# Kernel tuning notes

Hardware: AMD Instinct MI355X
Metric: run time of the kernel (lower is better)

The kernel has to match this reference:

```python
import jax, jax.numpy as jnp
import numpy as np

N_NODES = 50000
N_EDGES = 600000
F_IN = 64
N_GRAPHS = 2000
OUT_DIM = 1
BN_EPS = 1e-5


def _bn(x, gamma, beta):
    # BatchNorm1d training-mode forward: biased batch stats over node/row dim
    m = jnp.mean(x, axis=0)
    v = jnp.var(x, axis=0)
    return (x - m) * jax.lax.rsqrt(v + BN_EPS) * gamma + beta


def _gcn(x, W, b, src, dst):
    # PyG GCNConv: h = x @ W; symmetric-normalized aggregation with self-loops; bias after agg
    n = x.shape[0]
    h = x @ W                                    # [N, C_out]
    ones = jnp.ones((src.shape[0],), h.dtype)
    deg = jax.ops.segment_sum(ones, dst, num_segments=n) + 1.0  # +1 self-loop
    dinv = jax.lax.rsqrt(deg)
    norm = (dinv[src] * dinv[dst])[:, None]      # [E, 1]
    agg = jax.ops.segment_sum(h[src] * norm, dst, num_segments=n)
    agg = agg + h * (1.0 / deg)[:, None]         # self-loop term: deg^{-1/2}*deg^{-1/2}
    return agg + b


def _pool_mean(x, batch, g):
    s = jax.ops.segment_sum(x, batch, num_segments=g)
    c = jax.ops.segment_sum(jnp.ones((x.shape[0],), x.dtype), batch, num_segments=g)
    return s / jnp.maximum(c, 1.0)[:, None]


def _forward(xc, xs, W1c, b1c, g1c, be1c, W2c, b2c, g2c, be2c,
             W1s, b1s, g1s, be1s, W2s, b2s, g2s, be2s,
             Wf1, bf1, gf1, bef1, Wf2, bf2,
             src_c, dst_c, src_s, dst_s, batch):
    hc = jax.nn.relu(_bn(_gcn(xc, W1c, b1c, src_c, dst_c), g1c, be1c))
    hc = jax.nn.relu(_bn(_gcn(hc, W2c, b2c, src_c, dst_c), g2c, be2c))
    hs = jax.nn.relu(_bn(_gcn(xs, W1s, b1s, src_s, dst_s), g1s, be1s))
    hs = jax.nn.relu(_bn(_gcn(hs, W2s, b2s, src_s, dst_s), g2s, be2s))
    pc = _pool_mean(hc, batch, N_GRAPHS)         # [G, 64]
    ps = _pool_mean(hs, batch, N_GRAPHS)         # [G, 64]
    h = jnp.concatenate([pc, ps], axis=1)        # [G, 128]
    h = jax.nn.relu(_bn(h @ Wf1 + bf1, gf1, bef1))  # dropout is identity in eval
    return h @ Wf2 + bf2                         # [G, OUT_DIM]


def setup_inputs() -> dict:
    key = jax.random.key(0)
    ks = jax.random.split(key, 16)

    def glorot(k, fan_in, fan_out):
        s = np.sqrt(2.0 / (fan_in + fan_out)).astype(np.float32)
        return jax.random.normal(k, (fan_in, fan_out), jnp.float32) * s

    inp = {
        'x_chromophore': jax.random.normal(ks[0], (N_NODES, F_IN), jnp.float32),
        'x_solvent': jax.random.normal(ks[1], (N_NODES, F_IN), jnp.float32),
        'edge_index_chromophore': jax.random.randint(ks[2], (2, N_EDGES), 0, N_NODES),
        'edge_index_solvent': jax.random.randint(ks[3], (2, N_EDGES), 0, N_NODES),
        'batch': jnp.sort(jax.random.randint(ks[4], (N_NODES,), 0, N_GRAPHS)),
        # chromophore branch params
        'W1c': glorot(ks[5], F_IN, 128), 'b1c': jnp.zeros((128,), jnp.float32),
        'g1c': jnp.ones((128,), jnp.float32), 'be1c': jnp.zeros((128,), jnp.float32),
        'W2c': glorot(ks[6], 128, 64), 'b2c': jnp.zeros((64,), jnp.float32),
        'g2c': jnp.ones((64,), jnp.float32), 'be2c': jnp.zeros((64,), jnp.float32),
        # solvent branch params
        'W1s': glorot(ks[7], F_IN, 128), 'b1s': jnp.zeros((128,), jnp.float32),
        'g1s': jnp.ones((128,), jnp.float32), 'be1s': jnp.zeros((128,), jnp.float32),
        'W2s': glorot(ks[8], 128, 64), 'b2s': jnp.zeros((64,), jnp.float32),
        'g2s': jnp.ones((64,), jnp.float32), 'be2s': jnp.zeros((64,), jnp.float32),
        # MLP head
        'Wf1': glorot(ks[9], 128, 64), 'bf1': jnp.zeros((64,), jnp.float32),
        'gf1': jnp.ones((64,), jnp.float32), 'bef1': jnp.zeros((64,), jnp.float32),
        'Wf2': glorot(ks[10], 64, OUT_DIM), 'bf2': jnp.zeros((OUT_DIM,), jnp.float32),
    }
    return inp


def reference(x_chromophore, x_solvent, edge_index_chromophore, edge_index_solvent, batch,
              W1c, b1c, g1c, be1c, W2c, b2c, g2c, be2c,
              W1s, b1s, g1s, be1s, W2s, b2s, g2s, be2s,
              Wf1, bf1, gf1, bef1, Wf2, bf2):
    src_c, dst_c = edge_index_chromophore[0], edge_index_chromophore[1]
    src_s, dst_s = edge_index_solvent[0], edge_index_solvent[1]
    return _forward(x_chromophore, x_solvent,
                    W1c, b1c, g1c, be1c, W2c, b2c, g2c, be2c,
                    W1s, b1s, g1s, be1s, W2s, b2s, g2s, be2s,
                    Wf1, bf1, gf1, bef1, Wf2, bf2,
                    src_c, dst_c, src_s, dst_s, batch)
```

## Files before the change

kernel.cpp:

```cpp
#include <hip/hip_runtime.h>
#include <hip/hip_bf16.h>
#include <cstdint>
#include <cstddef>

#define NN 50000
#define NE 600000
#define NG 2000
#define NBUCK 49
#define SLOTS 16
#define NCHUNK 3125

typedef __attribute__((ext_vector_type(8))) short bf8;
typedef __attribute__((ext_vector_type(4))) float f32x4;

__device__ __forceinline__ unsigned short f2bf(float f) {
    uint32_t u = __float_as_uint(f);
    uint32_t r = (u + 0x7FFFu + ((u >> 16) & 1u)) >> 16;
    return (unsigned short)r;
}
__device__ __forceinline__ float bf2f(unsigned short h) {
    return __uint_as_float(((uint32_t)h) << 16);
}
__device__ __forceinline__ float lo16(uint32_t v) { return __uint_as_float(v << 16); }
__device__ __forceinline__ float hi16(uint32_t v) { return __uint_as_float(v & 0xFFFF0000u); }

__global__ __launch_bounds__(256) void conv_bf16_kernel(const float* __restrict__ x0,
                                                        const float* __restrict__ x1,
                                                        unsigned short* __restrict__ out) {
    int b = blockIdx.y;
    const float* x = b ? x1 : x0;
    unsigned short* o = out + (size_t)b * NN * 64;
    int i = (blockIdx.x * 256 + threadIdx.x) * 4;
    if (i + 3 < NN * 64) {
        float4 v = *(const float4*)&x[i];
        ushort4 r = make_ushort4(f2bf(v.x), f2bf(v.y), f2bf(v.z), f2bf(v.w));
        *(ushort4*)&o[i] = r;
    }
}

template<int K, int N>
__global__ __launch_bounds__(256) void pack_w(const float* __restrict__ W0,
                                              const float* __restrict__ W1,
                                              unsigned short* __restrict__ out) {
    int b = blockIdx.y;
    const float* W = b ? W1 : W0;
    unsigned short* o = out + (size_t)b * K * N;
    int idx = blockIdx.x * 256 + threadIdx.x;
    const int total = (N / 16) * (K / 32) * 64;
    if (idx >= total) return;
    int l = idx & 63;
    int th = idx >> 6;
    int h = th % (K / 32);
    int t = th / (K / 32);
    int col = t * 16 + (l & 15);
    int k0 = h * 32 + (l >> 4) * 8;
    ushort4 lo = make_ushort4(f2bf(W[(k0 + 0) * N + col]), f2bf(W[(k0 + 1) * N + col]),
                              f2bf(W[(k0 + 2) * N + col]), f2bf(W[(k0 + 3) * N + col]));
    ushort4 hi = make_ushort4(f2bf(W[(k0 + 4) * N + col]), f2bf(W[(k0 + 5) * N + col]),
                              f2bf(W[(k0 + 6) * N + col]), f2bf(W[(k0 + 7) * N + col]));
    *(ushort4*)&o[idx * 8] = lo;
    *(ushort4*)&o[idx * 8 + 4] = hi;
}

__global__ __launch_bounds__(256) void bucket_hist(const int* __restrict__ d0,
                                                   const int* __restrict__ d1,
                                                   int* __restrict__ bucketCnt, int nE) {
    int b = blockIdx.y;
    const int* dst = b ? d1 : d0;
    __shared__ int h[NBUCK];
    for (int i = threadIdx.x; i < NBUCK; i += 256) h[i] = 0;
    __syncthreads();
    for (int e = blockIdx.x * 256 + threadIdx.x; e < nE; e += gridDim.x * 256)
        atomicAdd(&h[dst[e] >> 10], 1);
    __syncthreads();
    for (int i = threadIdx.x; i < NBUCK; i += 256)
        if (h[i]) atomicAdd(&bucketCnt[b * NBUCK + i], h[i]);
}

__global__ void bucket_scan(const int* __restrict__ bucketCnt,
                            int* __restrict__ bucketOff, int* __restrict__ bucketCur) {
    int b = threadIdx.x;
    if (b < 2) {
        int run = 0;
        for (int i = 0; i < NBUCK; ++i) {
            bucketOff[b * NBUCK + i] = run;
            bucketCur[b * NBUCK + i] = run;
            run += bucketCnt[b * NBUCK + i];
        }
    }
}

__global__ __launch_bounds__(256) void bucket_scatter(const int* __restrict__ s0,
                                                      const int* __restrict__ d0,
                                                      const int* __restrict__ s1,
                                                      const int* __restrict__ d1,
                                                      int* __restrict__ bucketCur,
                                                      uint32_t* __restrict__ bent, int nE) {
    int b = blockIdx.y;
    const int* src = b ? s1 : s0;
    const int* dst = b ? d1 : d0;
    __shared__ int cnt[NBUCK];
    __shared__ int base[NBUCK];
    const int tid = threadIdx.x;
    for (int i = tid; i < NBUCK; i += 256) cnt[i] = 0;
    __syncthreads();

    const int e0 = blockIdx.x * 2048 + tid;
    int bk[8], slot[8];
    uint32_t pay[8];
#pragma unroll
    for (int k = 0; k < 8; ++k) {
        int e = e0 + k * 256;
        if (e < nE) {
            int d = dst[e], s = src[e];
            bk[k] = d >> 10;
            pay[k] = ((uint32_t)(d & 1023) << 16) | (uint32_t)s;
            slot[k] = atomicAdd(&cnt[bk[k]], 1);
        } else bk[k] = -1;
    }
    __syncthreads();
    for (int i = tid; i < NBUCK; i += 256) {
        int c = cnt[i];
        base[i] = c ? atomicAdd(&bucketCur[b * NBUCK + i], c) : 0;
    }
    __syncthreads();
#pragma unroll
    for (int k = 0; k < 8; ++k)
        if (bk[k] >= 0)
            bent[(size_t)b * NE + base[bk[k]] + slot[k]] = pay[k];
}

__global__ __launch_bounds__(256) void csr_build(const uint32_t* __restrict__ bent,
                                                 const int* __restrict__ bucketOff,
                                                 const int* __restrict__ bucketCnt,
                                                 int* __restrict__ row_ptr,
                                                 float* __restrict__ dinv,
                                                 uint16_t* __restrict__ perm) {
    __shared__ int lcnt[1024];
    __shared__ int lcur[1024];
    __shared__ int sscan[256];
    const int bk = blockIdx.x;
    const int b = blockIdx.y;
    const int tid = threadIdx.x;
    const int ebase = bucketOff[b * NBUCK + bk];
    const int ecnt = bucketCnt[b * NBUCK + bk];
    const int node0 = bk << 10;
    const uint32_t* be = bent + (size_t)b * NE + ebase;
    int* rp = row_ptr + b * (NN + 1);
    float* dv = dinv + (size_t)b * NN;
    uint16_t* pm = perm + (size_t)b * NE + ebase;

    for (int i = tid; i < 1024; i += 256) lcnt[i] = 0;
    __syncthreads();
    for (int i = tid; i < ecnt; i += 256) atomicAdd(&lcnt[be[i] >> 16], 1);
    __syncthreads();

    int c[4], s = 0;
#pragma unroll
    for (int j = 0; j < 4; ++j) { c[j] = lcnt[tid * 4 + j]; s += c[j]; }
    sscan[tid] = s;
    __syncthreads();
    for (int off = 1; off < 256; off <<= 1) {
        int v = (tid >= off) ? sscan[tid - off] : 0;
        __syncthreads();
        sscan[tid] += v;
        __syncthreads();
    }
    int run = sscan[tid] - s;
#pragma unroll
    for (int j = 0; j < 4; ++j) {
        int nl = tid * 4 + j;
        int g = node0 + nl;
        if (g < NN) {
            rp[g] = ebase + run;
            lcur[nl] = run;
            dv[g] = rsqrtf((float)c[j] + 1.0f);
        }
        run += c[j];
    }
    if (bk == NBUCK - 1 && tid == 0) rp[NN] = ebase + ecnt;
    __syncthreads();

    for (int i = tid; i < ecnt; i += 256) {
        uint32_t en = be[i];
        int nl = en >> 16;
        int pos = atomicAdd(&lcur[nl], 1);
        pm[pos] = (uint16_t)(en & 0xFFFFu);
    }
}

__global__ __launch_bounds__(256) void weight_fill(const uint16_t* __restrict__ perm,
                                                   const float* __restrict__ dinv,
                                                   uint32_t* __restrict__ permw, int nE) {
    int b = blockIdx.y;
    const uint16_t* pm = perm + (size_t)b * NE;
    const float* dv = dinv + (size_t)b * NN;
    uint32_t* pw = permw + (size_t)b * NE;
    int i = (blockIdx.x * 256 + threadIdx.x) * 4;
    if (i + 3 < nE) {
        ushort4 s4 = *(const ushort4*)&pm[i];
        uint4 o;
        o.x = ((uint32_t)f2bf(dv[s4.x]) << 16) | (uint32_t)s4.x;
        o.y = ((uint32_t)f2bf(dv[s4.y]) << 16) | (uint32_t)s4.y;
        o.z = ((uint32_t)f2bf(dv[s4.z]) << 16) | (uint32_t)s4.z;
        o.w = ((uint32_t)f2bf(dv[s4.w]) << 16) | (uint32_t)s4.w;
        *(uint4*)&pw[i] = o;
    } else {
        for (; i < nE; ++i) {
            uint16_t s = pm[i];
            pw[i] = ((uint32_t)f2bf(dv[s]) << 16) | (uint32_t)s;
        }
    }
}

__global__ __launch_bounds__(256) void graph_ranges(const int* __restrict__ batch,
                                                    int* __restrict__ gstart,
                                                    int* __restrict__ gend, int n) {
    int i = blockIdx.x * 256 + threadIdx.x;
    if (i >= n) return;
    int g = batch[i];
    if (i == 0 || batch[i - 1] != g) gstart[g] = i;
    if (i == n - 1 || batch[i + 1] != g) gend[g] = i + 1;
}

__global__ __launch_bounds__(256) void gemm1_mfma(const unsigned short* __restrict__ Xbf,
                                                  const unsigned short* __restrict__ Wp,
                                                  unsigned short* __restrict__ Y) {
    const int b = blockIdx.y;
    const unsigned short* __restrict__ X = Xbf + (size_t)b * NN * 64;
    const unsigned short* __restrict__ W = Wp + (size_t)b * 64 * 128;
    unsigned short* __restrict__ Yb = Y + (size_t)b * NN * 128;
    const int tid = threadIdx.x;
    const int w = tid >> 6, lane = tid & 63;
    const int chunk = blockIdx.x * 4 + w;
    if (chunk >= NCHUNK) return;
    const int m = lane & 15, quad = lane >> 4;

    const int row = chunk * 16 + m;
    bf8 a0 = *(const bf8*)&X[(size_t)row * 64 + quad * 8];
    bf8 a1 = *(const bf8*)&X[(size_t)row * 64 + 32 + quad * 8];
    f32x4 acc[8];
#pragma unroll
    for (int t = 0; t < 8; ++t) acc[t] = (f32x4){0.f, 0.f, 0.f, 0.f};
#pragma unroll
    for (int t = 0; t < 8; ++t) {
        bf8 b0 = *(const bf8*)&W[((t * 2 + 0) * 64 + lane) * 8];
        bf8 b1 = *(const bf8*)&W[((t * 2 + 1) * 64 + lane) * 8];
        acc[t] = __builtin_amdgcn_mfma_f32_16x16x32_bf16(b0, a0, acc[t], 0, 0, 0);
        acc[t] = __builtin_amdgcn_mfma_f32_16x16x32_bf16(b1, a1, acc[t], 0, 0, 0);
    }
#pragma unroll
    for (int t = 0; t < 8; ++t) {
        uint32_t lo = (uint32_t)f2bf(acc[t][0]) | ((uint32_t)f2bf(acc[t][1]) << 16);
        uint32_t hi = (uint32_t)f2bf(acc[t][2]) | ((uint32_t)f2bf(acc[t][3]) << 16);
        *(uint2*)&Yb[(size_t)row * 128 + t * 16 + quad * 4] = make_uint2(lo, hi);
    }
}

__global__ __launch_bounds__(256) void stats128_bf16(const unsigned short* __restrict__ Y,
                                                     float* __restrict__ sums) {
    const int b = blockIdx.y;
    const unsigned short* __restrict__ Yb = Y + (size_t)b * NN * 128;
    const int g = threadIdx.x & 31;
    const int rs = threadIdx.x >> 5;
    float s0 = 0.f, s1 = 0.f, s2 = 0.f, s3 = 0.f;
    float q0 = 0.f, q1 = 0.f, q2 = 0.f, q3 = 0.f;
    for (int r = blockIdx.x * 8 + rs; r < NN; r += gridDim.x * 8) {
        uint2 v = *(const uint2*)&Yb[(size_t)r * 128 + g * 4];
        float x0 = lo16(v.x);
        float x1 = hi16(v.x);
        float x2 = lo16(v.y);
        float x3 = hi16(v.y);
        s0 += x0; s1 += x1; s2 += x2; s3 += x3;
        q0 = fmaf(x0, x0, q0); q1 = fmaf(x1, x1, q1);
        q2 = fmaf(x2, x2, q2); q3 = fmaf(x3, x3, q3);
    }
    __shared__ float ls[8][128], lq[8][128];
    *(float4*)&ls[rs][g * 4] = make_float4(s0, s1, s2, s3);
    *(float4*)&lq[rs][g * 4] = make_float4(q0, q1, q2, q3);
    __syncthreads();
    if (threadIdx.x < 128) {
        const int c = threadIdx.x;
        float S = 0.f, Q = 0.f;
#pragma unroll
        for (int k = 0; k < 8; ++k) { S += ls[k][c]; Q += lq[k][c]; }
        int slot = blockIdx.x & (SLOTS - 1);
        float* sb = sums + (size_t)(b * SLOTS + slot) * 256;
        atomicAdd(&sb[c], S);
        atomicAdd(&sb[128 + c], Q);
    }
}

__global__ __launch_bounds__(256) void gemm2_mfma(const unsigned short* __restrict__ H1,
                                                  const unsigned short* __restrict__ Wp,
                                                  const float* __restrict__ sums,
                                                  const float* __restrict__ g0,
                                                  const float* __restrict__ g1,
                                                  const float* __restrict__ be0,
                                                  const float* __restrict__ be1,
                                                  unsigned short* __restrict__ Y) {
    __shared__ float scLds[128], shLds[128];
    const int b = blockIdx.y;
    const unsigned short* __restrict__ X = H1 + (size_t)b * NN * 128;
    const unsigned short* __restrict__ W = Wp + (size_t)b * 128 * 64;
    unsigned short* __restrict__ Yb = Y + (size_t)b * NN * 64;
    const int tid = threadIdx.x;

    if (tid < 128) {
        float s = 0.f, s2 = 0.f;
#pragma unroll
        for (int k = 0; k < SLOTS; ++k) {
            const float* sb = sums + (size_t)(b * SLOTS + k) * 256;
            s += sb[tid];
            s2 += sb[128 + tid];
        }
        const float invN = 1.0f / (float)NN;
        float mean = s * invN;
        float var = s2 * invN - mean * mean;
        float gamma = b ? g1[tid] : g0[tid];
        float beta = b ? be1[tid] : be0[tid];
        float sc = gamma * rsqrtf(var + 1e-5f);
        scLds[tid] = sc;
        shLds[tid] = beta - mean * sc;
    }
    __syncthreads();

    const int w = tid >> 6, lane = tid & 63;
    const int chunk = blockIdx.x * 4 + w;
    if (chunk >= NCHUNK) return;
    const int m = lane & 15, quad = lane >> 4;
    const int row = chunk * 16 + m;

    f32x4 acc[4];
#pragma unroll
    for (int t = 0; t < 4; ++t) acc[t] = (f32x4){0.f, 0.f, 0.f, 0.f};
#pragma unroll
    for (int h = 0; h < 4; ++h) {
        const int k0 = h * 32 + quad * 8;
        bf8 araw = *(const bf8*)&X[(size_t)row * 128 + k0];
        float4 sc0 = *(const float4*)&scLds[k0];
        float4 sc1 = *(const float4*)&scLds[k0 + 4];
        float4 sh0 = *(const float4*)&shLds[k0];
        float4 sh1 = *(const float4*)&shLds[k0 + 4];
        float scv[8] = {sc0.x, sc0.y, sc0.z, sc0.w, sc1.x, sc1.y, sc1.z, sc1.w};
        float shv[8] = {sh0.x, sh0.y, sh0.z, sh0.w, sh1.x, sh1.y, sh1.z, sh1.w};
        bf8 af;
#pragma unroll
        for (int j = 0; j < 8; ++j) {
            float v = bf2f((unsigned short)araw[j]);
            v = fmaxf(fmaf(v, scv[j], shv[j]), 0.f);
            af[j] = (short)f2bf(v);
        }
#pragma unroll
        for (int t = 0; t < 4; ++t) {
            bf8 bf = *(const bf8*)&W[((t * 4 + h) * 64 + lane) * 8];
            acc[t] = __builtin_amdgcn_mfma_f32_16x16x32_bf16(bf, af, acc[t], 0, 0, 0);
        }
    }
#pragma unroll
    for (int t = 0; t < 4; ++t) {
        uint32_t lo = (uint32_t)f2bf(acc[t][0]) | ((uint32_t)f2bf(acc[t][1]) << 16);
        uint32_t hi = (uint32_t)f2bf(acc[t][2]) | ((uint32_t)f2bf(acc[t][3]) << 16);
        *(uint2*)&Yb[(size_t)row * 64 + t * 16 + quad * 4] = make_uint2(lo, hi);
    }
}

template<bool STATS>
__global__ __launch_bounds__(256) void agg2_kernel(const unsigned short* __restrict__ hall,
                                                   const int* __restrict__ row_ptr,
                                                   const uint32_t* __restrict__ permw,
                                                   const float* __restrict__ dinv,
                                                   unsigned short* __restrict__ out,
                                                   float* __restrict__ sums, int nNodes) {
    const int bid = blockIdx.x;
    const int xcd = bid & 7;
    const int b = xcd >> 2;
    const int j = (bid >> 3) * 4 + (xcd & 3);
    const unsigned short* __restrict__ h = hall + (size_t)b * NN * 64;
    const int* rp = row_ptr + b * (NN + 1);
    const uint32_t* pe = permw + (size_t)b * NE;
    const float* dv = dinv + (size_t)b * NN;
    unsigned short* ob = out + (size_t)b * nNodes * 64;

    const int w = threadIdx.x >> 6;
    const int lane = threadIdx.x & 63;
    const int q = lane & 15;
    const int r = lane >> 4;
    const int d0 = j * 8 + w * 2;
    const int d1 = d0 + 1;
    const bool actA = d0 < nNodes;
    const bool actB = d1 < nNodes;

    float fA0 = 0.f, fA1 = 0.f, fA2 = 0.f, fA3 = 0.f;
    float fB0 = 0.f, fB1 = 0.f, fB2 = 0.f, fB3 = 0.f;
    int p0a = 0, p1a = 0, p0b = 0, p1b = 0;
    float dia = 0.f, dib = 0.f;
    if (actA) { p0a = rp[d0]; p1a = rp[d0 + 1]; dia = dv[d0]; }
    if (actB) { p0b = rp[d1]; p1b = rp[d1 + 1]; dib = dv[d1]; }

    float aA0 = 0.f, aA1 = 0.f, aA2 = 0.f, aA3 = 0.f;
    float aB0 = 0.f, aB1 = 0.f, aB2 = 0.f, aB3 = 0.f;
    int pa = p0a, pb = p0b;
    while (pa < p1a || pb < p1b) {
        uint32_t enA[4], enB[4];
#pragma unroll
        for (int k = 0; k < 4; ++k) {
            int e = pa + k * 4 + r;
            bool vld = e < p1a;
            enA[k] = pe[vld ? e : p0a];
            if (!vld) enA[k] &= 0xFFFFu;
        }
#pragma unroll
        for (int k = 0; k < 4; ++k) {
            int e = pb + k * 4 + r;
            bool vld = e < p1b;
            enB[k] = pe[vld ? e : p0b];
            if (!vld) enB[k] &= 0xFFFFu;
        }
#pragma unroll
        for (int k = 0; k < 4; ++k) {
            const int idx = (int)(enA[k] & 0xFFFFu);
            const float wk = __uint_as_float(enA[k] & 0xFFFF0000u);
            const uint2 hv = *(const uint2*)&h[(size_t)idx * 64 + q * 4];
            aA0 = fmaf(wk, lo16(hv.x), aA0);
            aA1 = fmaf(wk, hi16(hv.x), aA1);
            aA2 = fmaf(wk, lo16(hv.y), aA2);
            aA3 = fmaf(wk, hi16(hv.y), aA3);
        }
#pragma unroll
        for (int k = 0; k < 4; ++k) {
            const int idx = (int)(enB[k] & 0xFFFFu);
            const float wk = __uint_as_float(enB[k] & 0xFFFF0000u);
            const uint2 hv = *(const uint2*)&h[(size_t)idx * 64 + q * 4];
            aB0 = fmaf(wk, lo16(hv.x), aB0);
            aB1 = fmaf(wk, hi16(hv.x), aB1);
            aB2 = fmaf(wk, lo16(hv.y), aB2);
            aB3 = fmaf(wk, hi16(hv.y), aB3);
        }
        pa += 16;
        pb += 16;
    }
    aA0 += __shfl_xor(aA0, 16, 64); aA0 += __shfl_xor(aA0, 32, 64);
    aA1 += __shfl_xor(aA1, 16, 64); aA1 += __shfl_xor(aA1, 32, 64);
    aA2 += __shfl_xor(aA2, 16, 64); aA2 += __shfl_xor(aA2, 32, 64);
    aA3 += __shfl_xor(aA3, 16, 64); aA3 += __shfl_xor(aA3, 32, 64);
    aB0 += __shfl_xor(aB0, 16, 64); aB0 += __shfl_xor(aB0, 32, 64);
    aB1 += __shfl_xor(aB1, 16, 64); aB1 += __shfl_xor(aB1, 32, 64);
    aB2 += __shfl_xor(aB2, 16, 64); aB2 += __shfl_xor(aB2, 32, 64);
    aB3 += __shfl_xor(aB3, 16, 64); aB3 += __shfl_xor(aB3, 32, 64);

    if (actA) {
        const uint2 sv = *(const uint2*)&h[(size_t)d0 * 64 + q * 4];
        fA0 = dia * fmaf(dia, lo16(sv.x), aA0);
        fA1 = dia * fmaf(dia, hi16(sv.x), aA1);
        fA2 = dia * fmaf(dia, lo16(sv.y), aA2);
        fA3 = dia * fmaf(dia, hi16(sv.y), aA3);
        if (r == 0) {
            uint32_t o0 = (uint32_t)f2bf(fA0) | ((uint32_t)f2bf(fA1) << 16);
            uint32_t o1 = (uint32_t)f2bf(fA2) | ((uint32_t)f2bf(fA3) << 16);
            *(uint2*)&ob[(size_t)d0 * 64 + q * 4] = make_uint2(o0, o1);
        }
    }
    if (actB) {
        const uint2 sv = *(const uint2*)&h[(size_t)d1 * 64 + q * 4];
        fB0 = dib * fmaf(dib, lo16(sv.x), aB0);
        fB1 = dib * fmaf(dib, hi16(sv.x), aB1);
        fB2 = dib * fmaf(dib, lo16(sv.y), aB2);
        fB3 = dib * fmaf(dib, hi16(sv.y), aB3);
        if (r == 0) {
            uint32_t o0 = (uint32_t)f2bf(fB0) | ((uint32_t)f2bf(fB1) << 16);
            uint32_t o1 = (uint32_t)f2bf(fB2) | ((uint32_t)f2bf(fB3) << 16);
            *(uint2*)&ob[(size_t)d1 * 64 + q * 4] = make_uint2(o0, o1);
        }
    }
    if constexpr (STATS) {
        __shared__ float ls[256], ls2[256];
        if (lane < 16) {
            *(float4*)&ls[w * 64 + q * 4] =
                make_float4(fA0 + fB0, fA1 + fB1, fA2 + fB2, fA3 + fB3);
            *(float4*)&ls2[w * 64 + q * 4] =
                make_float4(fA0 * fA0 + fB0 * fB0, fA1 * fA1 + fB1 * fB1,
                            fA2 * fA2 + fB2 * fB2, fA3 * fA3 + fB3 * fB3);
        }
        __syncthreads();
        if (threadIdx.x < 64) {
            const int t = threadIdx.x;
            float s  = ls[t]  + ls[t + 64]  + ls[t + 128]  + ls[t + 192];
            float s2 = ls2[t] + ls2[t + 64] + ls2[t + 128] + ls2[t + 192];
            int slot = j & (SLOTS - 1);
            float* sb = sums + ((size_t)(b * SLOTS + slot) * 2) * 64;
            atomicAdd(&sb[t], s);
            atomicAdd(&sb[64 + t], s2);
        }
    }
}

__global__ __launch_bounds__(128) void pool_head_kernel(const unsigned short* __restrict__ x,
                                                        const float* __restrict__ sums,
                                                        const float* __restrict__ g0,
                                                        const float* __restrict__ g1,
                                                        const float* __restrict__ be0,
                                                        const float* __restrict__ be1,
                                                        const int* __restrict__ gstart,
                                                        const int* __restrict__ gend,
                                                        const float* __restrict__ Wf1,
                                                        float* __restrict__ T) {
    __shared__ float row[128];
    const int g = blockIdx.x;
    const int c = threadIdx.x;
    const int b = c >> 6;
    const int ch = c & 63;
    float s0 = 0.f, s20 = 0.f;
#pragma unroll
    for (int k = 0; k < SLOTS; ++k) {
        const float* sb = sums + ((size_t)(b * SLOTS + k) * 2) * 64;
        s0 += sb[ch];
        s20 += sb[64 + ch];
    }
    const float invN = 1.0f / (float)NN;
    float mean = s0 * invN;
    float var = s20 * invN - mean * mean;
    float gamma = b ? g1[ch] : g0[ch];
    float beta = b ? be1[ch] : be0[ch];
    float sc = gamma * rsqrtf(var + 1e-5f);
    float sh = beta - mean * sc;

    const unsigned short* xb = x + (size_t)b * NN * 64;
    const int start = gstart[g];
    const int end = gend[g];
    float s = 0.f;
    for (int r = start; r < end; ++r)
        s += fmaxf(fmaf(bf2f(xb[(size_t)r * 64 + ch]), sc, sh), 0.f);
    float cf = (float)(end - start);
    row[c] = s / fmaxf(cf, 1.f);
    __syncthreads();

    if (c < 64) {
        float acc = 0.f;
#pragma unroll 8
        for (int k = 0; k < 128; ++k) acc = fmaf(row[k], Wf1[k * 64 + c], acc);
        T[(size_t)g * 64 + c] = acc;
    }
}

template<int C>
__global__ __launch_bounds__(256) void bn_stats_kernel(const float* __restrict__ x, int n,
                                                       float* __restrict__ sums) {
    constexpr int RP = 256 / C;
    __shared__ float ls[256], ls2[256];
    int c = threadIdx.x % C;
    int sub = threadIdx.x / C;
    float s = 0.f, s2 = 0.f;
    for (int r = blockIdx.x * RP + sub; r < n; r += gridDim.x * RP) {
        float v = x[(size_t)r * C + c];
        s += v; s2 += v * v;
    }
    ls[threadIdx.x] = s; ls2[threadIdx.x] = s2;
    __syncthreads();
    if (sub == 0) {
#pragma unroll
        for (int k = 1; k < RP; ++k) { s += ls[k * C + c]; s2 += ls2[k * C + c]; }
        atomicAdd(&sums[c], s);
        atomicAdd(&sums[C + c], s2);
    }
}

__global__ __launch_bounds__(64) void head_final_kernel(const float* __restrict__ T,
                                                        const float* __restrict__ hsums,
                                                        const float* __restrict__ gf1,
                                                        const float* __restrict__ bef1,
                                                        const float* __restrict__ Wf2,
                                                        const float* __restrict__ bf2,
                                                        float* __restrict__ out) {
    int g = blockIdx.x;
    int c = threadIdx.x;
    const float invG = 1.0f / (float)NG;
    float mean = hsums[c] * invG;
    float var = hsums[64 + c] * invG - mean * mean;
    float sc = gf1[c] * rsqrtf(var + 1e-5f);
    float sh = bef1[c] - mean * sc;
    float v = fmaxf(fmaf(T[(size_t)g * 64 + c], sc, sh), 0.f) * Wf2[c];
#pragma unroll
    for (int off = 32; off > 0; off >>= 1) v += __shfl_down(v, off, 64);
    if (c == 0) out[g] = v + bf2[0];
}


static inline size_t alignup(size_t x) { return (x + 255) & ~(size_t)255; }

extern "C" void kernel_launch(void* const* d_in, const int* in_sizes, int n_in,
                              void* d_out, int out_size, void* d_ws, size_t ws_size,
                              hipStream_t stream) {
    const float* xc  = (const float*)d_in[0];
    const float* xs  = (const float*)d_in[1];
    const int*   eic = (const int*)d_in[2];
    const int*   eis = (const int*)d_in[3];
    const int*   batch = (const int*)d_in[4];
    const float* W1c = (const float*)d_in[5];
    const float* g1c = (const float*)d_in[7];
    const float* be1c = (const float*)d_in[8];
    const float* W2c = (const float*)d_in[9];
    const float* g2c = (const float*)d_in[11];
    const float* be2c = (const float*)d_in[12];
    const float* W1s = (const float*)d_in[13];
    const float* g1s = (const float*)d_in[15];
    const float* be1s = (const float*)d_in[16];
    const float* W2s = (const float*)d_in[17];
    const float* g2s = (const float*)d_in[19];
    const float* be2s = (const float*)d_in[20];
    const float* Wf1 = (const float*)d_in[21];
    const float* gf1 = (const float*)d_in[23];
    const float* bef1 = (const float*)d_in[24];
    const float* Wf2 = (const float*)d_in[25];
    const float* bf2 = (const float*)d_in[26];
    float* out = (float*)d_out;

    char* ws = (char*)d_ws;
    size_t off = 0;
    auto alloc = [&](size_t bytes) { char* p = ws + off; off += alignup(bytes); return p; };

    int*      bucketCnt = (int*)alloc(2 * NBUCK * 4);
    int*      bucketOff = (int*)alloc(2 * NBUCK * 4);
    int*      bucketCur = (int*)alloc(2 * NBUCK * 4);
    uint32_t* bent      = (uint32_t*)alloc((size_t)2 * NE * 4);
    uint16_t* perm      = (uint16_t*)alloc(((size_t)2 * NE + 64) * 2);
    int*      row_ptr   = (int*)alloc(2 * (NN + 1) * 4);
    float*    dinv      = (float*)alloc((size_t)2 * NN * 4);
    int*      gbound    = (int*)alloc((size_t)2 * NG * 4);
    unsigned short* xbf   = (unsigned short*)alloc((size_t)2 * NN * 64 * 2);
    unsigned short* aggbf = (unsigned short*)alloc((size_t)2 * NN * 64 * 2);
    unsigned short* h1bf  = (unsigned short*)alloc((size_t)2 * NN * 128 * 2);
    unsigned short* h2bf  = (unsigned short*)alloc((size_t)2 * NN * 64 * 2);
    unsigned short* Wp1   = (unsigned short*)alloc((size_t)2 * 64 * 128 * 2);
    unsigned short* Wp2   = (unsigned short*)alloc((size_t)2 * 128 * 64 * 2);
    float*    sums1     = (float*)alloc(((size_t)2 * SLOTS * 256 + (size_t)2 * SLOTS * 128 + 128) * 4);
    float*    sums2     = sums1 + (size_t)2 * SLOTS * 256;
    float*    hsums     = sums2 + (size_t)2 * SLOTS * 128;
    float*    T         = (float*)alloc((size_t)NG * 64 * 4);
    int*      gstart    = gbound;
    int*      gend      = gbound + NG;

    const size_t statBytes = ((size_t)2 * SLOTS * 256 + (size_t)2 * SLOTS * 128 + 128) * 4;
    const int gemmBlocks = (NCHUNK + 3) / 4;
    const int aggBlocks = 12504;

    conv_bf16_kernel<<<dim3((NN * 64 / 4 + 255) / 256, 2), 256, 0, stream>>>(xc, xs, xbf);
    pack_w<64, 128><<<dim3(4, 2), 256, 0, stream>>>(W1c, W1s, Wp1);
    pack_w<128, 64><<<dim3(4, 2), 256, 0, stream>>>(W2c, W2s, Wp2);
    hipMemsetAsync(sums1, 0, statBytes, stream);
    hipMemsetAsync(gbound, 0, 2 * NG * 4, stream);
    graph_ranges<<<(NN + 255) / 256, 256, 0, stream>>>(batch, gstart, gend, NN);

    hipMemsetAsync(bucketCnt, 0, 2 * NBUCK * 4, stream);
    bucket_hist<<<dim3(64, 2), 256, 0, stream>>>(eic + NE, eis + NE, bucketCnt, NE);
    bucket_scan<<<1, 64, 0, stream>>>(bucketCnt, bucketOff, bucketCur);
    bucket_scatter<<<dim3((NE + 2047) / 2048, 2), 256, 0, stream>>>(
        eic, eic + NE, eis, eis + NE, bucketCur, bent, NE);
    csr_build<<<dim3(NBUCK, 2), 256, 0, stream>>>(bent, bucketOff, bucketCnt,
                                                  row_ptr, dinv, perm);
    weight_fill<<<dim3((NE / 4 + 255) / 256, 2), 256, 0, stream>>>(perm, dinv, bent, NE);

    agg2_kernel<false><<<aggBlocks, 256, 0, stream>>>(
        xbf, row_ptr, bent, dinv, aggbf, nullptr, NN);
    gemm1_mfma<<<dim3(gemmBlocks, 2), 256, 0, stream>>>(aggbf, Wp1, h1bf);
    stats128_bf16<<<dim3(256, 2), 256, 0, stream>>>(h1bf, sums1);

    gemm2_mfma<<<dim3(gemmBlocks, 2), 256, 0, stream>>>(h1bf, Wp2, sums1,
                                                        g1c, g1s, be1c, be1s, h2bf);
    agg2_kernel<true><<<aggBlocks, 256, 0, stream>>>(
        h2bf, row_ptr, bent, dinv, aggbf, sums2, NN);

    pool_head_kernel<<<NG, 128, 0, stream>>>(aggbf, sums2, g2c, g2s, be2c, be2s,
                                             gstart, gend, Wf1, T);

    bn_stats_kernel<64><<<32, 256, 0, stream>>>(T, NG, hsums);
    head_final_kernel<<<NG, 64, 0, stream>>>(T, hsums, gf1, bef1, Wf2, bf2, out);
}
```

Before: 342.1 us.

## Merge prep launches, fuse BN stats into gemm1, binary-search graph ranges

```diff
diff --git a/kernel.cpp b/kernel.cpp
--- a/kernel.cpp
+++ b/kernel.cpp
@@ -24,28 +24,15 @@
 __device__ __forceinline__ float lo16(uint32_t v) { return __uint_as_float(v << 16); }
 __device__ __forceinline__ float hi16(uint32_t v) { return __uint_as_float(v & 0xFFFF0000u); }
 
-__global__ __launch_bounds__(256) void conv_bf16_kernel(const float* __restrict__ x0,
-                                                        const float* __restrict__ x1,
-                                                        unsigned short* __restrict__ out) {
-    int b = blockIdx.y;
-    const float* x = b ? x1 : x0;
-    unsigned short* o = out + (size_t)b * NN * 64;
-    int i = (blockIdx.x * 256 + threadIdx.x) * 4;
-    if (i + 3 < NN * 64) {
-        float4 v = *(const float4*)&x[i];
-        ushort4 r = make_ushort4(f2bf(v.x), f2bf(v.y), f2bf(v.z), f2bf(v.w));
-        *(ushort4*)&o[i] = r;
-    }
-}
-
-template<int K, int N>
-__global__ __launch_bounds__(256) void pack_w(const float* __restrict__ W0,
-                                              const float* __restrict__ W1,
-                                              unsigned short* __restrict__ out) {
-    int b = blockIdx.y;
-    const float* W = b ? W1 : W0;
-    unsigned short* o = out + (size_t)b * K * N;
-    int idx = blockIdx.x * 256 + threadIdx.x;
+#define PREP_CONV 6250
+#define PREP_P1   6258
+#define PREP_P2   6266
+#define PREP_ZS   6315
+#define PREP_TOT  6316
+
+__device__ __forceinline__ void pack_w_body(const float* __restrict__ W,
+                                            unsigned short* __restrict__ o,
+                                            int idx, int K, int N) {
     const int total = (N / 16) * (K / 32) * 64;
     if (idx >= total) return;
     int l = idx & 63;
@@ -60,6 +47,47 @@
                               f2bf(W[(k0 + 6) * N + col]), f2bf(W[(k0 + 7) * N + col]));
     *(ushort4*)&o[idx * 8] = lo;
     *(ushort4*)&o[idx * 8 + 4] = hi;
+}
+
+__global__ __launch_bounds__(256) void prep_kernel(const float* __restrict__ x0,
+                                                   const float* __restrict__ x1,
+                                                   unsigned short* __restrict__ xbf,
+                                                   const float* __restrict__ W1c,
+                                                   const float* __restrict__ W1s,
+                                                   unsigned short* __restrict__ Wp1,
+                                                   const float* __restrict__ W2c,
+                                                   const float* __restrict__ W2s,
+                                                   unsigned short* __restrict__ Wp2,
+                                                   float* __restrict__ sums,
+                                                   int* __restrict__ bucketCnt) {
+    const int bid = blockIdx.x;
+    const int tid = threadIdx.x;
+    if (bid < PREP_CONV) {
+        const int b = bid >= 3125;
+        const int lb = b ? bid - 3125 : bid;
+        const float* x = b ? x1 : x0;
+        unsigned short* o = xbf + (size_t)b * NN * 64;
+        int i = (lb * 256 + tid) * 4;
+        if (i + 3 < NN * 64) {
+            float4 v = *(const float4*)&x[i];
+            *(ushort4*)&o[i] = make_ushort4(f2bf(v.x), f2bf(v.y), f2bf(v.z), f2bf(v.w));
+        }
+    } else if (bid < PREP_P1) {
+        const int local = bid - PREP_CONV;
+        const int b = local >> 2;
+        pack_w_body(b ? W1s : W1c, Wp1 + (size_t)b * 64 * 128,
+                    (local & 3) * 256 + tid, 64, 128);
+    } else if (bid < PREP_P2) {
+        const int local = bid - PREP_P1;
+        const int b = local >> 2;
+        pack_w_body(b ? W2s : W2c, Wp2 + (size_t)b * 128 * 64,
+                    (local & 3) * 256 + tid, 128, 64);
+    } else if (bid < PREP_ZS) {
+        int i = (bid - PREP_P2) * 256 + tid;
+        if (i < 12416) sums[i] = 0.f;
+    } else {
+        if (tid < 2 * NBUCK) bucketCnt[tid] = 0;
+    }
 }
 
 __global__ __launch_bounds__(256) void bucket_hist(const int* __restrict__ d0,
@@ -213,19 +241,11 @@
     }
 }
 
-__global__ __launch_bounds__(256) void graph_ranges(const int* __restrict__ batch,
-                                                    int* __restrict__ gstart,
-                                                    int* __restrict__ gend, int n) {
-    int i = blockIdx.x * 256 + threadIdx.x;
-    if (i >= n) return;
-    int g = batch[i];
-    if (i == 0 || batch[i - 1] != g) gstart[g] = i;
-    if (i == n - 1 || batch[i + 1] != g) gend[g] = i + 1;
-}
-
 __global__ __launch_bounds__(256) void gemm1_mfma(const unsigned short* __restrict__ Xbf,
                                                   const unsigned short* __restrict__ Wp,
-                                                  unsigned short* __restrict__ Y) {
+                                                  unsigned short* __restrict__ Y,
+                                                  float* __restrict__ sums) {
+    __shared__ float ls[128], lq[128];
     const int b = blockIdx.y;
     const unsigned short* __restrict__ X = Xbf + (size_t)b * NN * 64;
     const unsigned short* __restrict__ W = Wp + (size_t)b * 64 * 128;
@@ -233,61 +253,50 @@
     const int tid = threadIdx.x;
     const int w = tid >> 6, lane = tid & 63;
     const int chunk = blockIdx.x * 4 + w;
-    if (chunk >= NCHUNK) return;
+    const bool act = chunk < NCHUNK;
     const int m = lane & 15, quad = lane >> 4;
 
-    const int row = chunk * 16 + m;
-    bf8 a0 = *(const bf8*)&X[(size_t)row * 64 + quad * 8];
-    bf8 a1 = *(const bf8*)&X[(size_t)row * 64 + 32 + quad * 8];
-    f32x4 acc[8];
-#pragma unroll
-    for (int t = 0; t < 8; ++t) acc[t] = (f32x4){0.f, 0.f, 0.f, 0.f};
-#pragma unroll
-    for (int t = 0; t < 8; ++t) {
-        bf8 b0 = *(const bf8*)&W[((t * 2 + 0) * 64 + lane) * 8];
-        bf8 b1 = *(const bf8*)&W[((t * 2 + 1) * 64 + lane) * 8];
-        acc[t] = __builtin_amdgcn_mfma_f32_16x16x32_bf16(b0, a0, acc[t], 0, 0, 0);
-        acc[t] = __builtin_amdgcn_mfma_f32_16x16x32_bf16(b1, a1, acc[t], 0, 0, 0);
-    }
-#pragma unroll
-    for (int t = 0; t < 8; ++t) {
-        uint32_t lo = (uint32_t)f2bf(acc[t][0]) | ((uint32_t)f2bf(acc[t][1]) << 16);
-        uint32_t hi = (uint32_t)f2bf(acc[t][2]) | ((uint32_t)f2bf(acc[t][3]) << 16);
-        *(uint2*)&Yb[(size_t)row * 128 + t * 16 + quad * 4] = make_uint2(lo, hi);
-    }
-}
-
-__global__ __launch_bounds__(256) void stats128_bf16(const unsigned short* __restrict__ Y,
-                                                     float* __restrict__ sums) {
-    const int b = blockIdx.y;
-    const unsigned short* __restrict__ Yb = Y + (size_t)b * NN * 128;
-    const int g = threadIdx.x & 31;
-    const int rs = threadIdx.x >> 5;
-    float s0 = 0.f, s1 = 0.f, s2 = 0.f, s3 = 0.f;
-    float q0 = 0.f, q1 = 0.f, q2 = 0.f, q3 = 0.f;
-    for (int r = blockIdx.x * 8 + rs; r < NN; r += gridDim.x * 8) {
-        uint2 v = *(const uint2*)&Yb[(size_t)r * 128 + g * 4];
-        float x0 = lo16(v.x);
-        float x1 = hi16(v.x);
-        float x2 = lo16(v.y);
-        float x3 = hi16(v.y);
-        s0 += x0; s1 += x1; s2 += x2; s3 += x3;
-        q0 = fmaf(x0, x0, q0); q1 = fmaf(x1, x1, q1);
-        q2 = fmaf(x2, x2, q2); q3 = fmaf(x3, x3, q3);
-    }
-    __shared__ float ls[8][128], lq[8][128];
-    *(float4*)&ls[rs][g * 4] = make_float4(s0, s1, s2, s3);
-    *(float4*)&lq[rs][g * 4] = make_float4(q0, q1, q2, q3);
-    __syncthreads();
-    if (threadIdx.x < 128) {
-        const int c = threadIdx.x;
-        float S = 0.f, Q = 0.f;
-#pragma unroll
-        for (int k = 0; k < 8; ++k) { S += ls[k][c]; Q += lq[k][c]; }
+    if (tid < 128) { ls[tid] = 0.f; lq[tid] = 0.f; }
+    __syncthreads();
+
+    if (act) {
+        const int row = chunk * 16 + m;
+        bf8 a0 = *(const bf8*)&X[(size_t)row * 64 + quad * 8];
+        bf8 a1 = *(const bf8*)&X[(size_t)row * 64 + 32 + quad * 8];
+        f32x4 acc[8];
+#pragma unroll
+        for (int t = 0; t < 8; ++t) acc[t] = (f32x4){0.f, 0.f, 0.f, 0.f};
+#pragma unroll
+        for (int t = 0; t < 8; ++t) {
+            bf8 b0 = *(const bf8*)&W[((t * 2 + 0) * 64 + lane) * 8];
+            bf8 b1 = *(const bf8*)&W[((t * 2 + 1) * 64 + lane) * 8];
+            acc[t] = __builtin_amdgcn_mfma_f32_16x16x32_bf16(b0, a0, acc[t], 0, 0, 0);
+            acc[t] = __builtin_amdgcn_mfma_f32_16x16x32_bf16(b1, a1, acc[t], 0, 0, 0);
+        }
+#pragma unroll
+        for (int t = 0; t < 8; ++t) {
+            uint32_t lo = (uint32_t)f2bf(acc[t][0]) | ((uint32_t)f2bf(acc[t][1]) << 16);
+            uint32_t hi = (uint32_t)f2bf(acc[t][2]) | ((uint32_t)f2bf(acc[t][3]) << 16);
+            *(uint2*)&Yb[(size_t)row * 128 + t * 16 + quad * 4] = make_uint2(lo, hi);
+        }
+#pragma unroll
+        for (int tt = 0; tt < 8; ++tt) {
+            const int t = (tt + m) & 7;
+            const int ch = t * 16 + quad * 4;
+#pragma unroll
+            for (int r = 0; r < 4; ++r) {
+                const float v = acc[t][r];
+                atomicAdd(&ls[ch + r], v);
+                atomicAdd(&lq[ch + r], v * v);
+            }
+        }
+    }
+    __syncthreads();
+    if (tid < 128) {
         int slot = blockIdx.x & (SLOTS - 1);
         float* sb = sums + (size_t)(b * SLOTS + slot) * 256;
-        atomicAdd(&sb[c], S);
-        atomicAdd(&sb[128 + c], Q);
+        atomicAdd(&sb[tid], ls[tid]);
+        atomicAdd(&sb[128 + tid], lq[tid]);
     }
 }
 
@@ -501,10 +510,9 @@
                                                         const float* __restrict__ g1,
                                                         const float* __restrict__ be0,
                                                         const float* __restrict__ be1,
-                                                        const int* __restrict__ gstart,
-                                                        const int* __restrict__ gend,
+                                                        const int* __restrict__ batch,
                                                         const float* __restrict__ Wf1,
-                                                        float* __restrict__ T) {
+                                                        float* __restrict__ T, int n) {
     __shared__ float row[128];
     const int g = blockIdx.x;
     const int c = threadIdx.x;
@@ -525,9 +533,14 @@
     float sc = gamma * rsqrtf(var + 1e-5f);
     float sh = beta - mean * sc;
 
+    int lo = 0, hi = n;
+    while (lo < hi) { int mid = (lo + hi) >> 1; if (batch[mid] < g) lo = mid + 1; else hi = mid; }
+    const int start = lo;
+    hi = n;
+    while (lo < hi) { int mid = (lo + hi) >> 1; if (batch[mid] <= g) lo = mid + 1; else hi = mid; }
+    const int end = lo;
+
     const unsigned short* xb = x + (size_t)b * NN * 64;
-    const int start = gstart[g];
-    const int end = gend[g];
     float s = 0.f;
     for (int r = start; r < end; ++r)
         s += fmaxf(fmaf(bf2f(xb[(size_t)r * 64 + ch]), sc, sh), 0.f);
@@ -626,7 +639,6 @@
     uint16_t* perm      = (uint16_t*)alloc(((size_t)2 * NE + 64) * 2);
     int*      row_ptr   = (int*)alloc(2 * (NN + 1) * 4);
     float*    dinv      = (float*)alloc((size_t)2 * NN * 4);
-    int*      gbound    = (int*)alloc((size_t)2 * NG * 4);
     unsigned short* xbf   = (unsigned short*)alloc((size_t)2 * NN * 64 * 2);
     unsigned short* aggbf = (unsigned short*)alloc((size_t)2 * NN * 64 * 2);
     unsigned short* h1bf  = (unsigned short*)alloc((size_t)2 * NN * 128 * 2);
@@ -637,21 +649,13 @@
     float*    sums2     = sums1 + (size_t)2 * SLOTS * 256;
     float*    hsums     = sums2 + (size_t)2 * SLOTS * 128;
     float*    T         = (float*)alloc((size_t)NG * 64 * 4);
-    int*      gstart    = gbound;
-    int*      gend      = gbound + NG;
-
-    const size_t statBytes = ((size_t)2 * SLOTS * 256 + (size_t)2 * SLOTS * 128 + 128) * 4;
+
     const int gemmBlocks = (NCHUNK + 3) / 4;
     const int aggBlocks = 12504;
 
-    conv_bf16_kernel<<<dim3((NN * 64 / 4 + 255) / 256, 2), 256, 0, stream>>>(xc, xs, xbf);
-    pack_w<64, 128><<<dim3(4, 2), 256, 0, stream>>>(W1c, W1s, Wp1);
-    pack_w<128, 64><<<dim3(4, 2), 256, 0, stream>>>(W2c, W2s, Wp2);
-    hipMemsetAsync(sums1, 0, statBytes, stream);
-    hipMemsetAsync(gbound, 0, 2 * NG * 4, stream);
-    graph_ranges<<<(NN + 255) / 256, 256, 0, stream>>>(batch, gstart, gend, NN);
-
-    hipMemsetAsync(bucketCnt, 0, 2 * NBUCK * 4, stream);
+    prep_kernel<<<PREP_TOT, 256, 0, stream>>>(xc, xs, xbf, W1c, W1s, Wp1,
+                                              W2c, W2s, Wp2, sums1, bucketCnt);
+
     bucket_hist<<<dim3(64, 2), 256, 0, stream>>>(eic + NE, eis + NE, bucketCnt, NE);
     bucket_scan<<<1, 64, 0, stream>>>(bucketCnt, bucketOff, bucketCur);
     bucket_scatter<<<dim3((NE + 2047) / 2048, 2), 256, 0, stream>>>(
@@ -662,8 +666,7 @@
 
     agg2_kernel<false><<<aggBlocks, 256, 0, stream>>>(
         xbf, row_ptr, bent, dinv, aggbf, nullptr, NN);
-    gemm1_mfma<<<dim3(gemmBlocks, 2), 256, 0, stream>>>(aggbf, Wp1, h1bf);
-    stats128_bf16<<<dim3(256, 2), 256, 0, stream>>>(h1bf, sums1);
+    gemm1_mfma<<<dim3(gemmBlocks, 2), 256, 0, stream>>>(aggbf, Wp1, h1bf, sums1);
 
     gemm2_mfma<<<dim3(gemmBlocks, 2), 256, 0, stream>>>(h1bf, Wp2, sums1,
                                                         g1c, g1s, be1c, be1s, h2bf);
@@ -671,7 +674,7 @@
         h2bf, row_ptr, bent, dinv, aggbf, sums2, NN);
 
     pool_head_kernel<<<NG, 128, 0, stream>>>(aggbf, sums2, g2c, g2s, be2c, be2s,
-                                             gstart, gend, Wf1, T);
+                                             batch, Wf1, T, NN);
 
     bn_stats_kernel<64><<<32, 256, 0, stream>>>(T, NG, hsums);
     head_final_kernel<<<NG, 64, 0, stream>>>(T, hsums, gf1, bef1, Wf2, bf2, out);
```

After: 456.8 us. +33.5%, slower.
